# Kernel optimization log

Measured on AMD Instinct MI355X. Metric: run time of the kernel, lower is better.

## Reference

```python
import jax, jax.numpy as jnp
import numpy as np
from jax import lax

B, N_PROP, N_GT = 8, 8000, 256
NUM_CLASSES = 2
IMG_H = IMG_W = 800.0
FG_T = BG_T = 0.5            # Matcher thresholds
WX, WY, WW, WH = 10.0, 10.0, 5.0, 5.0  # BoxCoder weights
SCORE_T, NMS_T = 0.05, 0.5
PRE_NMS, DETS = 1000, 300     # boxes entering NMS, detections_per_img
DW_CLIP = float(np.log(1000.0 / 16.0))


def _rand_boxes(key, shape):
    k1, k2, k3, k4 = jax.random.split(key, 4)
    x1 = jax.random.uniform(k1, shape) * (IMG_W - 60.0)
    y1 = jax.random.uniform(k2, shape) * (IMG_H - 60.0)
    w = 10.0 + jax.random.uniform(k3, shape) * 250.0
    h = 10.0 + jax.random.uniform(k4, shape) * 250.0
    return jnp.stack([x1, y1, jnp.minimum(x1 + w, IMG_W), jnp.minimum(y1 + h, IMG_H)], -1)


def setup_inputs() -> dict:
    key = jax.random.key(0)
    kp, kg, kl, kb = jax.random.split(key, 4)
    n_all = N_PROP + N_GT
    return {
        "proposals": _rand_boxes(kp, (B, N_PROP)),
        "gt_boxes": _rand_boxes(kg, (B, N_GT)),
        "logits": jax.random.normal(kl, (B, n_all, NUM_CLASSES), jnp.float32),
        "box_regression": jax.random.normal(kb, (B, n_all, NUM_CLASSES * 4), jnp.float32) * 0.1,
    }


def box_iou(a, b):
    # a: [Na,4], b: [Nb,4] in xyxy -> [Na,Nb]
    area_a = (a[:, 2] - a[:, 0]) * (a[:, 3] - a[:, 1])
    area_b = (b[:, 2] - b[:, 0]) * (b[:, 3] - b[:, 1])
    lt = jnp.maximum(a[:, None, :2], b[None, :, :2])
    rb = jnp.minimum(a[:, None, 2:], b[None, :, 2:])
    wh = jnp.clip(rb - lt, 0.0)
    inter = wh[..., 0] * wh[..., 1]
    return inter / (area_a[:, None] + area_b[None, :] - inter)


def encode(ref_boxes, gt):
    # BoxCoder.encode, weights (10,10,5,5)
    pw = ref_boxes[:, 2] - ref_boxes[:, 0]
    ph = ref_boxes[:, 3] - ref_boxes[:, 1]
    pcx = ref_boxes[:, 0] + 0.5 * pw
    pcy = ref_boxes[:, 1] + 0.5 * ph
    gw = gt[:, 2] - gt[:, 0]
    gh = gt[:, 3] - gt[:, 1]
    gcx = gt[:, 0] + 0.5 * gw
    gcy = gt[:, 1] + 0.5 * gh
    return jnp.stack([
        WX * (gcx - pcx) / pw,
        WY * (gcy - pcy) / ph,
        WW * jnp.log(gw / pw),
        WH * jnp.log(gh / ph),
    ], -1)


def decode(rel, boxes):
    # rel: [N, C*4], boxes: [N,4] -> [N, C, 4]
    rel = rel.reshape(rel.shape[0], -1, 4)
    pw = boxes[:, 2] - boxes[:, 0]
    ph = boxes[:, 3] - boxes[:, 1]
    pcx = boxes[:, 0] + 0.5 * pw
    pcy = boxes[:, 1] + 0.5 * ph
    dx = rel[..., 0] / WX
    dy = rel[..., 1] / WY
    dw = jnp.minimum(rel[..., 2] / WW, DW_CLIP)
    dh = jnp.minimum(rel[..., 3] / WH, DW_CLIP)
    cx = dx * pw[:, None] + pcx[:, None]
    cy = dy * ph[:, None] + pcy[:, None]
    w = jnp.exp(dw) * pw[:, None]
    h = jnp.exp(dh) * ph[:, None]
    return jnp.stack([cx - 0.5 * w, cy - 0.5 * h, cx + 0.5 * w, cy + 0.5 * h], -1)


def _per_image(prop, gt, logit, breg):
    n_all = prop.shape[0] + gt.shape[0]
    prop_all = jnp.concatenate([prop, gt], 0)  # select_training_samples concat

    # --- assign_targets_to_proposals (Matcher) ---
    iou = box_iou(gt, prop_all)                 # [G, N_all]
    vals = iou.max(0)
    matches = iou.argmax(0)
    # gt_labels are all 1; bg -> 0, between thresholds -> -1 (empty when fg==bg)
    labels = jnp.where(vals < BG_T, 0, jnp.where(vals < FG_T, -1, 1))
    matched_gt = gt[matches]                    # [N_all, 4]
    reg_targets = encode(prop_all, matched_gt)  # [N_all, 4]

    # --- postprocess_detections ---
    pred = decode(breg, prop_all)               # [N_all, C, 4]
    boxes1 = pred[:, 1, :]                      # drop background class
    boxes1 = jnp.stack([
        jnp.clip(boxes1[:, 0], 0.0, IMG_W),
        jnp.clip(boxes1[:, 1], 0.0, IMG_H),
        jnp.clip(boxes1[:, 2], 0.0, IMG_W),
        jnp.clip(boxes1[:, 3], 0.0, IMG_H),
    ], -1)
    scores = jax.nn.softmax(logit, -1)[:, 1]
    sc = jnp.where(scores > SCORE_T, scores, -1.0)  # score_thresh filter

    top_s, top_i = lax.top_k(sc, PRE_NMS)
    top_b = boxes1[top_i]                       # [M, 4]
    ious = box_iou(top_b, top_b)                # [M, M]
    idx = jnp.arange(PRE_NMS)

    def body(keep, i):
        sup = (ious[i] > NMS_T) & keep[i] & (idx > i)
        return keep & ~sup, None

    keep, _ = lax.scan(body, jnp.ones(PRE_NMS, bool), idx)
    final = jnp.where(keep & (top_s > 0.0), top_s, -1.0)
    det_s, sel = lax.top_k(final, DETS)
    det_b = top_b[sel]
    return labels.astype(jnp.float32), reg_targets, det_b, det_s


def reference(proposals, gt_boxes, logits, box_regression):
    return jax.vmap(_per_image)(proposals, gt_boxes, logits, box_regression)
```

## Files before the change

kernel.cpp:

```cpp
#include <hip/hip_runtime.h>
#include <math.h>

#pragma clang fp contract(off)

#define BATCH 8
#define N_PROP 8000
#define N_GT 256
#define N_ALL 8256
#define PRE_NMS 1000
#define DETS 300
#define IMG 800.0f
#define DW_CLIP 4.135166556742356f
#define NWORDS 32
#define NBINS 8192
#define BIN_SCALE 8192.0f

__device__ __forceinline__ float exf(float x) { return (float)exp((double)x); }
__device__ __forceinline__ float lgf(float x) { return (float)log((double)x); }

__device__ __forceinline__ int score_bin(float s) {
  int b = (int)(s * BIN_SCALE);
  return (b < 0) ? 0 : (b > NBINS - 1 ? NBINS - 1 : b);
}

__device__ __forceinline__ int bxp(int j) { return j ^ ((j >> 5) & 7); }

#define REP32(F) F(0) F(1) F(2) F(3) F(4) F(5) F(6) F(7) F(8) F(9) F(10) \
  F(11) F(12) F(13) F(14) F(15) F(16) F(17) F(18) F(19) F(20) F(21) F(22) \
  F(23) F(24) F(25) F(26) F(27) F(28) F(29) F(30) F(31)


__global__ void __launch_bounds__(256)
prep_kernel(const float* __restrict__ prop,
            const float* __restrict__ gt,
            const float* __restrict__ logits,
            const float* __restrict__ breg,
            float* __restrict__ out_labels,
            float* __restrict__ out_regt,
            float* __restrict__ ws_boxes1,
            float* __restrict__ ws_sc) {
  const int b = blockIdx.y;
  const int tid = threadIdx.x;
  __shared__ __align__(16) float4 gsh4[N_GT];
  __shared__ float s_best[32];
  __shared__ int s_bi[32];
  {
    const float4* g4 = (const float4*)(gt + (size_t)b * N_GT * 4);
    gsh4[tid] = g4[tid];
  }
  __syncthreads();

  const int grp = tid >> 3;
  const int gl  = tid & 7;
  const int j = blockIdx.x * 32 + grp;

  float x1, y1, x2, y2;
  if (j < N_PROP) {
    const float4 p = ((const float4*)(prop + (size_t)b * N_PROP * 4))[j];
    x1 = p.x; y1 = p.y; x2 = p.z; y2 = p.w;
  } else {
    const float4 g = gsh4[j - N_PROP];
    x1 = g.x; y1 = g.y; x2 = g.z; y2 = g.w;
  }
  const float areaP = (x2 - x1) * (y2 - y1);

  float best = -1.0f; int bi = gl;
  #pragma unroll 4
  for (int t = 0; t < 32; ++t) {
    const int i = gl + (t << 3);
    const float4 g = gsh4[i];
    const float ga = (g.z - g.x) * (g.w - g.y);
    const float w = fmaxf(fminf(g.z, x2) - fmaxf(g.x, x1), 0.0f);
    const float h = fmaxf(fminf(g.w, y2) - fmaxf(g.y, y1), 0.0f);
    const float inter = w * h;
    const float iou = inter / (ga + areaP - inter);
    if (iou > best) { best = iou; bi = i; }
  }
  #pragma unroll
  for (int m = 1; m < 8; m <<= 1) {
    const float ov = __shfl_xor(best, m, 64);
    const int   oi = __shfl_xor(bi,  m, 64);
    if (ov > best || (ov == best && oi < bi)) { best = ov; bi = oi; }
  }
  if (gl == 0) { s_best[grp] = best; s_bi[grp] = bi; }
  __syncthreads();

  if (tid < 32) {
    const int j2 = blockIdx.x * 32 + tid;
    const float bst = s_best[tid];
    const int   gi  = s_bi[tid];

    float px1, py1, px2, py2;
    if (j2 < N_PROP) {
      const float4 p = ((const float4*)(prop + (size_t)b * N_PROP * 4))[j2];
      px1 = p.x; py1 = p.y; px2 = p.z; py2 = p.w;
    } else {
      const float4 g = gsh4[j2 - N_PROP];
      px1 = g.x; py1 = g.y; px2 = g.z; py2 = g.w;
    }

    out_labels[(size_t)b * N_ALL + j2] = (bst < 0.5f) ? 0.0f : 1.0f;

    const float pw = px2 - px1, ph = py2 - py1;
    const float pcx = px1 + 0.5f * pw, pcy = py1 + 0.5f * ph;
    const float4 gb = gsh4[gi];
    const float gw = gb.z - gb.x, gh = gb.w - gb.y;
    const float gcx = gb.x + 0.5f * gw, gcy = gb.y + 0.5f * gh;
    float4 rt;
    rt.x = 10.0f * (gcx - pcx) / pw;
    rt.y = 10.0f * (gcy - pcy) / ph;
    rt.z = 5.0f * lgf(gw / pw);
    rt.w = 5.0f * lgf(gh / ph);
    ((float4*)out_regt)[(size_t)b * N_ALL + j2] = rt;

    const float4 r = *(const float4*)(breg + (((size_t)b * N_ALL + j2) * 8 + 4));
    const float dx = r.x / 10.0f, dy = r.y / 10.0f;
    const float dw = fminf(r.z / 5.0f, DW_CLIP);
    const float dh = fminf(r.w / 5.0f, DW_CLIP);
    const float cx = dx * pw + pcx, cy = dy * ph + pcy;
    const float w2 = exf(dw) * pw, h2 = exf(dh) * ph;
    float4 bb;
    bb.x = fminf(fmaxf(cx - 0.5f * w2, 0.0f), IMG);
    bb.y = fminf(fmaxf(cy - 0.5f * h2, 0.0f), IMG);
    bb.z = fminf(fmaxf(cx + 0.5f * w2, 0.0f), IMG);
    bb.w = fminf(fmaxf(cy + 0.5f * h2, 0.0f), IMG);
    ((float4*)ws_boxes1)[(size_t)b * N_ALL + j2] = bb;

    const float2 lg = *(const float2*)(logits + ((size_t)b * N_ALL + j2) * 2);
    const float m = fmaxf(lg.x, lg.y);
    const float e0 = exf(lg.x - m), e1 = exf(lg.y - m);
    const float s = e1 / (e0 + e1);
    ws_sc[(size_t)b * N_ALL + j2] = (s > 0.05f) ? s : -1.0f;
  }
}

__global__ void __launch_bounds__(1024)
select_rank_kernel(const float* __restrict__ ws_sc,
                   const float* __restrict__ ws_boxes1,
                   float* __restrict__ top_s,
                   float* __restrict__ top_b) {
  const int b = blockIdx.x;
  const int tid = threadIdx.x;
  const int lane = tid & 63, wid = tid >> 6;
  __shared__ __align__(16) float ssc[N_ALL];
  __shared__ unsigned hist[NBINS];
  __shared__ __align__(16) float sc2[N_ALL];
  __shared__ unsigned short idx2[N_ALL];
  __shared__ int s_wt[16], s_wx[16];
  __shared__ int s_T, s_Nc;

  {
    const float4* g = (const float4*)(ws_sc + (size_t)b * N_ALL);
    float4* s4 = (float4*)ssc;
    float4 a0 = g[tid], a1 = g[tid + 1024];
    float4 a2 = make_float4(0.f, 0.f, 0.f, 0.f);
    const bool g2 = (tid + 2048) < (N_ALL / 4);
    if (g2) a2 = g[tid + 2048];
    s4[tid] = a0; s4[tid + 1024] = a1;
    if (g2) s4[tid + 2048] = a2;
  }
  #pragma unroll
  for (int i = 0; i < NBINS / 1024; ++i) hist[tid + i * 1024] = 0u;
  __syncthreads();
  for (int k = tid; k < N_ALL; k += 1024)
    atomicAdd(&hist[score_bin(ssc[k])], 1u);
  __syncthreads();

  int local = 0;
  #pragma unroll
  for (int i = 0; i < NBINS / 1024; ++i) local += (int)hist[tid * (NBINS / 1024) + i];

  int incl = local;
  #pragma unroll
  for (int off = 1; off < 64; off <<= 1) {
    const int u = __shfl_down(incl, off);
    incl += (lane + off < 64) ? u : 0;
  }
  if (lane == 0) s_wt[wid] = incl;
  __syncthreads();
  if (tid < 16) {
    const int v = s_wt[tid];
    int inc2 = v;
    #pragma unroll
    for (int off = 1; off < 16; off <<= 1) {
      const int u = __shfl_down(inc2, off);
      inc2 += (tid + off < 16) ? u : 0;
    }
    s_wx[tid] = inc2 - v;
  }
  __syncthreads();
  const int sa = (incl - local) + s_wx[wid];

  {
    int above = sa;
    const int hi = tid * (NBINS / 1024) + (NBINS / 1024) - 1;
    #pragma unroll
    for (int i = 0; i < NBINS / 1024; ++i) {
      const int bin = hi - i;
      const int c = (int)hist[bin];
      if (above < PRE_NMS && above + c >= PRE_NMS) { s_T = bin; s_Nc = above + c; }
      hist[bin] = (unsigned)above;
      above += c;
    }
  }
  __syncthreads();
  const int T = s_T;
  const int Nc = s_Nc;

  for (int k = tid; k < N_ALL; k += 1024) {
    const float v = ssc[k];
    const int bb = score_bin(v);
    if (bb >= T) {
      const int slot = (int)atomicAdd(&hist[bb], 1u);
      sc2[slot] = v;
      idx2[slot] = (unsigned short)k;
    }
  }
  __syncthreads();

  float* tsb = top_s + (size_t)b * PRE_NMS;
  float4* tbb = (float4*)top_b + (size_t)b * PRE_NMS;
  const float4* bx = (const float4*)ws_boxes1 + (size_t)b * N_ALL;
  for (int s = tid; s < Nc; s += 1024) {
    const float my = sc2[s];
    const int myb = score_bin(my);
    const int myi = (int)idx2[s];
    int gl = s;
    while (gl > 0 && score_bin(sc2[gl - 1]) == myb) --gl;
    int rank = gl;
    for (int k2 = gl; k2 < Nc; ++k2) {
      const float v = sc2[k2];
      if (score_bin(v) != myb) break;
      if (k2 == s) continue;
      rank += (int)((v > my) | ((v == my) & ((int)idx2[k2] < myi)));
    }
    if (rank < PRE_NMS) {
      tsb[rank] = my;
      tbb[rank] = bx[myi];
    }
  }
}

__global__ void mask_kernel(const float* __restrict__ top_b,
                            unsigned* __restrict__ ws_mask) {
  const int b = blockIdx.y;
  __shared__ __align__(16) float4 bx[PRE_NMS];
  const int tid = threadIdx.x;
  {
    const float4* gb = (const float4*)top_b + (size_t)b * PRE_NMS;
    float4 v0 = gb[tid], v1 = gb[tid + 256], v2 = gb[tid + 512];
    float4 v3 = make_float4(0.f, 0.f, 0.f, 0.f);
    const bool g3 = (tid + 768) < PRE_NMS;
    if (g3) v3 = gb[tid + 768];
    bx[bxp(tid)] = v0; bx[bxp(tid + 256)] = v1; bx[bxp(tid + 512)] = v2;
    if (g3) bx[bxp(tid + 768)] = v3;
  }
  __syncthreads();
  const int idx = blockIdx.x * blockDim.x + tid;
  if (idx >= PRE_NMS * NWORDS) return;
  const int i = idx >> 5;
  const int w = idx & 31;
  const float4 bi = bx[bxp(i)];
  const float ai = (bi.z - bi.x) * (bi.w - bi.y);
  unsigned bits = 0u;
  const int j0 = w * 32;
  #pragma unroll 8
  for (int jj = 0; jj < 32; ++jj) {
    const int j = j0 + jj;
    if (j > i && j < PRE_NMS) {
      const float4 bj = bx[bxp(j)];
      const float aj = (bj.z - bj.x) * (bj.w - bj.y);
      const float ww = fmaxf(fminf(bi.z, bj.z) - fmaxf(bi.x, bj.x), 0.0f);
      const float hh = fmaxf(fminf(bi.w, bj.w) - fmaxf(bi.y, bj.y), 0.0f);
      const float inter = ww * hh;
      const float iou = inter / (ai + aj - inter);
      if (iou > 0.5f) bits |= (1u << jj);
    }
  }
  ws_mask[((size_t)b * PRE_NMS + i) * NWORDS + w] = bits;
}

__global__ void __launch_bounds__(256)
scan_kernel(const unsigned* __restrict__ ws_mask,
            const float* __restrict__ top_s,
            const float* __restrict__ top_b,
            float* __restrict__ out_detb,
            float* __restrict__ out_dets) {
  const int b = blockIdx.x;
  const int tid = threadIdx.x;
  __shared__ __align__(16) unsigned smask[PRE_NMS * NWORDS];
  __shared__ int s_npos;
  __shared__ unsigned s_flw[NWORDS];
  __shared__ int s_pref[NWORDS + 1];
  const float* ts = top_s + (size_t)b * PRE_NMS;

  if (tid == 0) s_npos = 0;
  {
    const uint4* gm = (const uint4*)(ws_mask + (size_t)b * PRE_NMS * NWORDS);
    uint4* sm4 = (uint4*)smask;
    #pragma unroll
    for (int gs = 0; gs < 4; ++gs) {
      const int k0 = gs * 2048 + tid;
      uint4 t0 = gm[k0],        t1 = gm[k0 + 256],  t2 = gm[k0 + 512];
      uint4 t3 = gm[k0 + 768],  t4 = gm[k0 + 1024], t5 = gm[k0 + 1280];
      uint4 t6 = gm[k0 + 1536];
      uint4 t7 = make_uint4(0u, 0u, 0u, 0u);
      const bool g7 = (k0 + 1792) < (PRE_NMS * NWORDS / 4);
      if (g7) t7 = gm[k0 + 1792];
      sm4[k0] = t0;        sm4[k0 + 256] = t1;  sm4[k0 + 512] = t2;
      sm4[k0 + 768] = t3;  sm4[k0 + 1024] = t4; sm4[k0 + 1280] = t5;
      sm4[k0 + 1536] = t6;
      if (g7) sm4[k0 + 1792] = t7;
    }
  }
  int cnt = 0;
  for (int k = tid; k < PRE_NMS; k += 256) cnt += (ts[k] > 0.0f) ? 1 : 0;
  __syncthreads();
  if (cnt) atomicAdd(&s_npos, cnt);

  unsigned keep = 0u;
  if (tid < 64) {
    const int lane = tid;
    const int lw = lane & 31;
    keep = (lane < NWORDS) ? ((lane == 31) ? 0xFFu : 0xFFFFFFFFu) : 0u;
#define DECLA(J) unsigned rA##J;
    REP32(DECLA)
#undef DECLA
    for (int win = 0; win < 32; ++win) {
      const int base = win * 32;
#define LOADA(J) rA##J = smask[(base + J) * NWORDS + lw];
      REP32(LOADA)
#undef LOADA
      unsigned sw = (unsigned)__builtin_amdgcn_readlane((int)keep, win);
      unsigned sup = 0u;
#define STEPJ(J) { \
      const unsigned mJ = 0u - ((sw >> J) & 1u); \
      const unsigned rwJ = (unsigned)__builtin_amdgcn_readlane((int)rA##J, win); \
      sw &= ~(rwJ & mJ); \
      sup |= (rA##J & mJ); }
      REP32(STEPJ)
#undef STEPJ
      keep &= ~sup;
    }
  }
  __syncthreads();
  const int n_pos = s_npos;
  if (tid < NWORDS) {
    const int lo = tid * 32;
    int np = n_pos - lo;
    np = (np < 0) ? 0 : (np > 32 ? 32 : np);
    const unsigned npm = (np >= 32) ? 0xFFFFFFFFu : ((1u << np) - 1u);
    s_flw[tid] = keep & npm;
  }
  __syncthreads();
  if (tid == 0) {
    int s = 0;
    #pragma unroll
    for (int w = 0; w < NWORDS; ++w) { s_pref[w] = s; s += __popc(s_flw[w]); }
    s_pref[NWORDS] = s;
  }
  __syncthreads();
  const int tot = s_pref[NWORDS];

  for (int k = tid; k < PRE_NMS; k += 256) {
    const unsigned fw = s_flw[k >> 5];
    const int fbit = (int)((fw >> (k & 31)) & 1u);
    const int pos = s_pref[k >> 5] + __popc(fw & ((1u << (k & 31)) - 1u));
    int slot = -1; float sval = 0.0f;
    if (fbit) {
      if (pos < DETS) { slot = pos; sval = ts[k]; }
    } else {
      const int s2 = tot + (k - pos);
      if (s2 < DETS) { slot = s2; sval = -1.0f; }
    }
    if (slot >= 0) {
      out_dets[(size_t)b * DETS + slot] = sval;
      ((float4*)out_detb)[(size_t)b * DETS + slot] =
          ((const float4*)top_b)[(size_t)b * PRE_NMS + k];
    }
  }
}

extern "C" void kernel_launch(void* const* d_in, const int* in_sizes, int n_in,
                              void* d_out, int out_size, void* d_ws, size_t ws_size,
                              hipStream_t stream) {
  const float* prop   = (const float*)d_in[0];
  const float* gt     = (const float*)d_in[1];
  const float* logits = (const float*)d_in[2];
  const float* breg   = (const float*)d_in[3];

  float* out        = (float*)d_out;
  float* out_labels = out;
  float* out_regt   = out + (size_t)BATCH * N_ALL;
  float* out_detb   = out_regt + (size_t)BATCH * N_ALL * 4;
  float* out_dets   = out_detb + (size_t)BATCH * DETS * 4;

  float* ws_boxes1 = (float*)d_ws;
  float* ws_sc     = ws_boxes1 + (size_t)BATCH * N_ALL * 4;
  float* ws_tops   = ws_sc + (size_t)BATCH * N_ALL;
  float* ws_topb   = ws_tops + (size_t)BATCH * PRE_NMS;
  unsigned* ws_mask = (unsigned*)(ws_topb + (size_t)BATCH * PRE_NMS * 4);

  hipLaunchKernelGGL(prep_kernel, dim3(258, BATCH), dim3(256), 0, stream,
                     prop, gt, logits, breg, out_labels, out_regt, ws_boxes1, ws_sc);
  hipLaunchKernelGGL(select_rank_kernel, dim3(BATCH), dim3(1024), 0, stream,
                     ws_sc, ws_boxes1, ws_tops, ws_topb);
  dim3 gridm((PRE_NMS * NWORDS + 255) / 256, BATCH);
  hipLaunchKernelGGL(mask_kernel, gridm, dim3(256), 0, stream,
                     ws_topb, ws_mask);
  hipLaunchKernelGGL(scan_kernel, dim3(BATCH), dim3(256), 0, stream,
                     ws_mask, ws_tops, ws_topb, out_detb, out_dets);
}
```

Measured before the change: 65.09 us.

## Fuse score/decode into select kernel and co-schedule matcher with mask kernel

Softmax scoring moves into the select/rank kernel, and box decoding is done only for the top-ranked boxes there. This removes the prep kernel's full-size workspace writes and the separate launch. The matcher/encode work now runs as extra blocks inside the NMS mask kernel, so it overlaps with mask computation and drops another launch. The NMS scan also skips windows whose keep word is already zero. The cost is more serial work in the 8-block select kernel, which now reads the logits directly.

```diff
diff --git a/kernel.cpp b/kernel.cpp
--- a/kernel.cpp
+++ b/kernel.cpp
@@ -14,6 +14,8 @@
 #define NWORDS 32
 #define NBINS 8192
 #define BIN_SCALE 8192.0f
+#define MASK_BLOCKS 125
+#define PREP_BLOCKS 258
 
 __device__ __forceinline__ float exf(float x) { return (float)exp((double)x); }
 __device__ __forceinline__ float lgf(float x) { return (float)log((double)x); }
@@ -30,113 +32,11 @@
   F(23) F(24) F(25) F(26) F(27) F(28) F(29) F(30) F(31)
 
 
-__global__ void __launch_bounds__(256)
-prep_kernel(const float* __restrict__ prop,
-            const float* __restrict__ gt,
-            const float* __restrict__ logits,
-            const float* __restrict__ breg,
-            float* __restrict__ out_labels,
-            float* __restrict__ out_regt,
-            float* __restrict__ ws_boxes1,
-            float* __restrict__ ws_sc) {
-  const int b = blockIdx.y;
-  const int tid = threadIdx.x;
-  __shared__ __align__(16) float4 gsh4[N_GT];
-  __shared__ float s_best[32];
-  __shared__ int s_bi[32];
-  {
-    const float4* g4 = (const float4*)(gt + (size_t)b * N_GT * 4);
-    gsh4[tid] = g4[tid];
-  }
-  __syncthreads();
-
-  const int grp = tid >> 3;
-  const int gl  = tid & 7;
-  const int j = blockIdx.x * 32 + grp;
-
-  float x1, y1, x2, y2;
-  if (j < N_PROP) {
-    const float4 p = ((const float4*)(prop + (size_t)b * N_PROP * 4))[j];
-    x1 = p.x; y1 = p.y; x2 = p.z; y2 = p.w;
-  } else {
-    const float4 g = gsh4[j - N_PROP];
-    x1 = g.x; y1 = g.y; x2 = g.z; y2 = g.w;
-  }
-  const float areaP = (x2 - x1) * (y2 - y1);
-
-  float best = -1.0f; int bi = gl;
-  #pragma unroll 4
-  for (int t = 0; t < 32; ++t) {
-    const int i = gl + (t << 3);
-    const float4 g = gsh4[i];
-    const float ga = (g.z - g.x) * (g.w - g.y);
-    const float w = fmaxf(fminf(g.z, x2) - fmaxf(g.x, x1), 0.0f);
-    const float h = fmaxf(fminf(g.w, y2) - fmaxf(g.y, y1), 0.0f);
-    const float inter = w * h;
-    const float iou = inter / (ga + areaP - inter);
-    if (iou > best) { best = iou; bi = i; }
-  }
-  #pragma unroll
-  for (int m = 1; m < 8; m <<= 1) {
-    const float ov = __shfl_xor(best, m, 64);
-    const int   oi = __shfl_xor(bi,  m, 64);
-    if (ov > best || (ov == best && oi < bi)) { best = ov; bi = oi; }
-  }
-  if (gl == 0) { s_best[grp] = best; s_bi[grp] = bi; }
-  __syncthreads();
-
-  if (tid < 32) {
-    const int j2 = blockIdx.x * 32 + tid;
-    const float bst = s_best[tid];
-    const int   gi  = s_bi[tid];
-
-    float px1, py1, px2, py2;
-    if (j2 < N_PROP) {
-      const float4 p = ((const float4*)(prop + (size_t)b * N_PROP * 4))[j2];
-      px1 = p.x; py1 = p.y; px2 = p.z; py2 = p.w;
-    } else {
-      const float4 g = gsh4[j2 - N_PROP];
-      px1 = g.x; py1 = g.y; px2 = g.z; py2 = g.w;
-    }
-
-    out_labels[(size_t)b * N_ALL + j2] = (bst < 0.5f) ? 0.0f : 1.0f;
-
-    const float pw = px2 - px1, ph = py2 - py1;
-    const float pcx = px1 + 0.5f * pw, pcy = py1 + 0.5f * ph;
-    const float4 gb = gsh4[gi];
-    const float gw = gb.z - gb.x, gh = gb.w - gb.y;
-    const float gcx = gb.x + 0.5f * gw, gcy = gb.y + 0.5f * gh;
-    float4 rt;
-    rt.x = 10.0f * (gcx - pcx) / pw;
-    rt.y = 10.0f * (gcy - pcy) / ph;
-    rt.z = 5.0f * lgf(gw / pw);
-    rt.w = 5.0f * lgf(gh / ph);
-    ((float4*)out_regt)[(size_t)b * N_ALL + j2] = rt;
-
-    const float4 r = *(const float4*)(breg + (((size_t)b * N_ALL + j2) * 8 + 4));
-    const float dx = r.x / 10.0f, dy = r.y / 10.0f;
-    const float dw = fminf(r.z / 5.0f, DW_CLIP);
-    const float dh = fminf(r.w / 5.0f, DW_CLIP);
-    const float cx = dx * pw + pcx, cy = dy * ph + pcy;
-    const float w2 = exf(dw) * pw, h2 = exf(dh) * ph;
-    float4 bb;
-    bb.x = fminf(fmaxf(cx - 0.5f * w2, 0.0f), IMG);
-    bb.y = fminf(fmaxf(cy - 0.5f * h2, 0.0f), IMG);
-    bb.z = fminf(fmaxf(cx + 0.5f * w2, 0.0f), IMG);
-    bb.w = fminf(fmaxf(cy + 0.5f * h2, 0.0f), IMG);
-    ((float4*)ws_boxes1)[(size_t)b * N_ALL + j2] = bb;
-
-    const float2 lg = *(const float2*)(logits + ((size_t)b * N_ALL + j2) * 2);
-    const float m = fmaxf(lg.x, lg.y);
-    const float e0 = exf(lg.x - m), e1 = exf(lg.y - m);
-    const float s = e1 / (e0 + e1);
-    ws_sc[(size_t)b * N_ALL + j2] = (s > 0.05f) ? s : -1.0f;
-  }
-}
-
 __global__ void __launch_bounds__(1024)
-select_rank_kernel(const float* __restrict__ ws_sc,
-                   const float* __restrict__ ws_boxes1,
+select_rank_kernel(const float* __restrict__ prop,
+                   const float* __restrict__ gt,
+                   const float* __restrict__ logits,
+                   const float* __restrict__ breg,
                    float* __restrict__ top_s,
                    float* __restrict__ top_b) {
   const int b = blockIdx.x;
@@ -146,18 +46,18 @@
   __shared__ unsigned hist[NBINS];
   __shared__ __align__(16) float sc2[N_ALL];
   __shared__ unsigned short idx2[N_ALL];
+  __shared__ __align__(16) float4 gsh[N_GT];
   __shared__ int s_wt[16], s_wx[16];
   __shared__ int s_T, s_Nc;
 
-  {
-    const float4* g = (const float4*)(ws_sc + (size_t)b * N_ALL);
-    float4* s4 = (float4*)ssc;
-    float4 a0 = g[tid], a1 = g[tid + 1024];
-    float4 a2 = make_float4(0.f, 0.f, 0.f, 0.f);
-    const bool g2 = (tid + 2048) < (N_ALL / 4);
-    if (g2) a2 = g[tid + 2048];
-    s4[tid] = a0; s4[tid + 1024] = a1;
-    if (g2) s4[tid + 2048] = a2;
+  if (tid < N_GT) gsh[tid] = ((const float4*)(gt + (size_t)b * N_GT * 4))[tid];
+
+  for (int k = tid; k < N_ALL; k += 1024) {
+    const float2 lg = *(const float2*)(logits + ((size_t)b * N_ALL + k) * 2);
+    const float m = fmaxf(lg.x, lg.y);
+    const float e0 = exf(lg.x - m), e1 = exf(lg.y - m);
+    const float s = e1 / (e0 + e1);
+    ssc[k] = (s > 0.05f) ? s : -1.0f;
   }
   #pragma unroll
   for (int i = 0; i < NBINS / 1024; ++i) hist[tid + i * 1024] = 0u;
@@ -220,7 +120,6 @@
 
   float* tsb = top_s + (size_t)b * PRE_NMS;
   float4* tbb = (float4*)top_b + (size_t)b * PRE_NMS;
-  const float4* bx = (const float4*)ws_boxes1 + (size_t)b * N_ALL;
   for (int s = tid; s < Nc; s += 1024) {
     const float my = sc2[s];
     const int myb = score_bin(my);
@@ -236,48 +135,144 @@
     }
     if (rank < PRE_NMS) {
       tsb[rank] = my;
-      tbb[rank] = bx[myi];
+      float4 pb;
+      if (myi < N_PROP) pb = ((const float4*)(prop + (size_t)b * N_PROP * 4))[myi];
+      else              pb = gsh[myi - N_PROP];
+      const float pw = pb.z - pb.x, ph = pb.w - pb.y;
+      const float pcx = pb.x + 0.5f * pw, pcy = pb.y + 0.5f * ph;
+      const float4 r = *(const float4*)(breg + (((size_t)b * N_ALL + myi) * 8 + 4));
+      const float dx = r.x / 10.0f, dy = r.y / 10.0f;
+      const float dw = fminf(r.z / 5.0f, DW_CLIP);
+      const float dh = fminf(r.w / 5.0f, DW_CLIP);
+      const float cx = dx * pw + pcx, cy = dy * ph + pcy;
+      const float w2 = exf(dw) * pw, h2 = exf(dh) * ph;
+      float4 bb;
+      bb.x = fminf(fmaxf(cx - 0.5f * w2, 0.0f), IMG);
+      bb.y = fminf(fmaxf(cy - 0.5f * h2, 0.0f), IMG);
+      bb.z = fminf(fmaxf(cx + 0.5f * w2, 0.0f), IMG);
+      bb.w = fminf(fmaxf(cy + 0.5f * h2, 0.0f), IMG);
+      tbb[rank] = bb;
     }
   }
 }
 
-__global__ void mask_kernel(const float* __restrict__ top_b,
-                            unsigned* __restrict__ ws_mask) {
+__global__ void __launch_bounds__(256)
+mask_prep_kernel(const float* __restrict__ prop,
+                 const float* __restrict__ gt,
+                 const float* __restrict__ top_b,
+                 unsigned* __restrict__ ws_mask,
+                 float* __restrict__ out_labels,
+                 float* __restrict__ out_regt) {
   const int b = blockIdx.y;
+  const int tid = threadIdx.x;
   __shared__ __align__(16) float4 bx[PRE_NMS];
-  const int tid = threadIdx.x;
-  {
-    const float4* gb = (const float4*)top_b + (size_t)b * PRE_NMS;
-    float4 v0 = gb[tid], v1 = gb[tid + 256], v2 = gb[tid + 512];
-    float4 v3 = make_float4(0.f, 0.f, 0.f, 0.f);
-    const bool g3 = (tid + 768) < PRE_NMS;
-    if (g3) v3 = gb[tid + 768];
-    bx[bxp(tid)] = v0; bx[bxp(tid + 256)] = v1; bx[bxp(tid + 512)] = v2;
-    if (g3) bx[bxp(tid + 768)] = v3;
-  }
-  __syncthreads();
-  const int idx = blockIdx.x * blockDim.x + tid;
-  if (idx >= PRE_NMS * NWORDS) return;
-  const int i = idx >> 5;
-  const int w = idx & 31;
-  const float4 bi = bx[bxp(i)];
-  const float ai = (bi.z - bi.x) * (bi.w - bi.y);
-  unsigned bits = 0u;
-  const int j0 = w * 32;
-  #pragma unroll 8
-  for (int jj = 0; jj < 32; ++jj) {
-    const int j = j0 + jj;
-    if (j > i && j < PRE_NMS) {
-      const float4 bj = bx[bxp(j)];
-      const float aj = (bj.z - bj.x) * (bj.w - bj.y);
-      const float ww = fmaxf(fminf(bi.z, bj.z) - fmaxf(bi.x, bj.x), 0.0f);
-      const float hh = fmaxf(fminf(bi.w, bj.w) - fmaxf(bi.y, bj.y), 0.0f);
-      const float inter = ww * hh;
-      const float iou = inter / (ai + aj - inter);
-      if (iou > 0.5f) bits |= (1u << jj);
-    }
-  }
-  ws_mask[((size_t)b * PRE_NMS + i) * NWORDS + w] = bits;
+  __shared__ __align__(16) float4 gsh4[N_GT];
+  __shared__ float s_best[32];
+  __shared__ int s_bi[32];
+
+  if (blockIdx.x < MASK_BLOCKS) {
+    {
+      const float4* gb = (const float4*)top_b + (size_t)b * PRE_NMS;
+      float4 v0 = gb[tid], v1 = gb[tid + 256], v2 = gb[tid + 512];
+      float4 v3 = make_float4(0.f, 0.f, 0.f, 0.f);
+      const bool g3 = (tid + 768) < PRE_NMS;
+      if (g3) v3 = gb[tid + 768];
+      bx[bxp(tid)] = v0; bx[bxp(tid + 256)] = v1; bx[bxp(tid + 512)] = v2;
+      if (g3) bx[bxp(tid + 768)] = v3;
+    }
+    __syncthreads();
+    const int idx = blockIdx.x * 256 + tid;
+    const int i = idx >> 5;
+    const int w = idx & 31;
+    const float4 bi = bx[bxp(i)];
+    const float ai = (bi.z - bi.x) * (bi.w - bi.y);
+    unsigned bits = 0u;
+    const int j0 = w * 32;
+    #pragma unroll 8
+    for (int jj = 0; jj < 32; ++jj) {
+      const int j = j0 + jj;
+      if (j > i && j < PRE_NMS) {
+        const float4 bj = bx[bxp(j)];
+        const float aj = (bj.z - bj.x) * (bj.w - bj.y);
+        const float ww = fmaxf(fminf(bi.z, bj.z) - fmaxf(bi.x, bj.x), 0.0f);
+        const float hh = fmaxf(fminf(bi.w, bj.w) - fmaxf(bi.y, bj.y), 0.0f);
+        const float inter = ww * hh;
+        const float iou = inter / (ai + aj - inter);
+        if (iou > 0.5f) bits |= (1u << jj);
+      }
+    }
+    ws_mask[((size_t)b * PRE_NMS + i) * NWORDS + w] = bits;
+  } else {
+    {
+      const float4* g4 = (const float4*)(gt + (size_t)b * N_GT * 4);
+      gsh4[tid] = g4[tid];
+    }
+    __syncthreads();
+
+    const int grp = tid >> 3;
+    const int gl  = tid & 7;
+    const int j = (blockIdx.x - MASK_BLOCKS) * 32 + grp;
+
+    float x1, y1, x2, y2;
+    if (j < N_PROP) {
+      const float4 p = ((const float4*)(prop + (size_t)b * N_PROP * 4))[j];
+      x1 = p.x; y1 = p.y; x2 = p.z; y2 = p.w;
+    } else {
+      const float4 g = gsh4[j - N_PROP];
+      x1 = g.x; y1 = g.y; x2 = g.z; y2 = g.w;
+    }
+    const float areaP = (x2 - x1) * (y2 - y1);
+
+    float best = -1.0f; int bi = gl;
+    #pragma unroll 4
+    for (int t = 0; t < 32; ++t) {
+      const int i = gl + (t << 3);
+      const float4 g = gsh4[i];
+      const float ga = (g.z - g.x) * (g.w - g.y);
+      const float w = fmaxf(fminf(g.z, x2) - fmaxf(g.x, x1), 0.0f);
+      const float h = fmaxf(fminf(g.w, y2) - fmaxf(g.y, y1), 0.0f);
+      const float inter = w * h;
+      const float iou = inter / (ga + areaP - inter);
+      if (iou > best) { best = iou; bi = i; }
+    }
+    #pragma unroll
+    for (int m = 1; m < 8; m <<= 1) {
+      const float ov = __shfl_xor(best, m, 64);
+      const int   oi = __shfl_xor(bi,  m, 64);
+      if (ov > best || (ov == best && oi < bi)) { best = ov; bi = oi; }
+    }
+    if (gl == 0) { s_best[grp] = best; s_bi[grp] = bi; }
+    __syncthreads();
+
+    if (tid < 32) {
+      const int j2 = (blockIdx.x - MASK_BLOCKS) * 32 + tid;
+      const float bst = s_best[tid];
+      const int   gi  = s_bi[tid];
+
+      float px1, py1, px2, py2;
+      if (j2 < N_PROP) {
+        const float4 p = ((const float4*)(prop + (size_t)b * N_PROP * 4))[j2];
+        px1 = p.x; py1 = p.y; px2 = p.z; py2 = p.w;
+      } else {
+        const float4 g = gsh4[j2 - N_PROP];
+        px1 = g.x; py1 = g.y; px2 = g.z; py2 = g.w;
+      }
+
+      out_labels[(size_t)b * N_ALL + j2] = (bst < 0.5f) ? 0.0f : 1.0f;
+
+      const float pw = px2 - px1, ph = py2 - py1;
+      const float pcx = px1 + 0.5f * pw, pcy = py1 + 0.5f * ph;
+      const float4 gb = gsh4[gi];
+      const float gw = gb.z - gb.x, gh = gb.w - gb.y;
+      const float gcx = gb.x + 0.5f * gw, gcy = gb.y + 0.5f * gh;
+      float4 rt;
+      rt.x = 10.0f * (gcx - pcx) / pw;
+      rt.y = 10.0f * (gcy - pcy) / ph;
+      rt.z = 5.0f * lgf(gw / pw);
+      rt.w = 5.0f * lgf(gh / ph);
+      ((float4*)out_regt)[(size_t)b * N_ALL + j2] = rt;
+    }
+  }
 }
 
 __global__ void __launch_bounds__(256)
@@ -327,20 +322,22 @@
     REP32(DECLA)
 #undef DECLA
     for (int win = 0; win < 32; ++win) {
-      const int base = win * 32;
+      unsigned sw = (unsigned)__builtin_amdgcn_readlane((int)keep, win);
+      if (sw) {
+        const int base = win * 32;
 #define LOADA(J) rA##J = smask[(base + J) * NWORDS + lw];
-      REP32(LOADA)
+        REP32(LOADA)
 #undef LOADA
-      unsigned sw = (unsigned)__builtin_amdgcn_readlane((int)keep, win);
-      unsigned sup = 0u;
+        unsigned sup = 0u;
 #define STEPJ(J) { \
-      const unsigned mJ = 0u - ((sw >> J) & 1u); \
-      const unsigned rwJ = (unsigned)__builtin_amdgcn_readlane((int)rA##J, win); \
-      sw &= ~(rwJ & mJ); \
-      sup |= (rA##J & mJ); }
-      REP32(STEPJ)
+        const unsigned mJ = 0u - ((sw >> J) & 1u); \
+        const unsigned rwJ = (unsigned)__builtin_amdgcn_readlane((int)rA##J, win); \
+        sw &= ~(rwJ & mJ); \
+        sup |= (rA##J & mJ); }
+        REP32(STEPJ)
 #undef STEPJ
-      keep &= ~sup;
+        keep &= ~sup;
+      }
     }
   }
   __syncthreads();
@@ -395,19 +392,15 @@
   float* out_detb   = out_regt + (size_t)BATCH * N_ALL * 4;
   float* out_dets   = out_detb + (size_t)BATCH * DETS * 4;
 
-  float* ws_boxes1 = (float*)d_ws;
-  float* ws_sc     = ws_boxes1 + (size_t)BATCH * N_ALL * 4;
-  float* ws_tops   = ws_sc + (size_t)BATCH * N_ALL;
+  float* ws_tops   = (float*)d_ws;
   float* ws_topb   = ws_tops + (size_t)BATCH * PRE_NMS;
   unsigned* ws_mask = (unsigned*)(ws_topb + (size_t)BATCH * PRE_NMS * 4);
 
-  hipLaunchKernelGGL(prep_kernel, dim3(258, BATCH), dim3(256), 0, stream,
-                     prop, gt, logits, breg, out_labels, out_regt, ws_boxes1, ws_sc);
   hipLaunchKernelGGL(select_rank_kernel, dim3(BATCH), dim3(1024), 0, stream,
-                     ws_sc, ws_boxes1, ws_tops, ws_topb);
-  dim3 gridm((PRE_NMS * NWORDS + 255) / 256, BATCH);
-  hipLaunchKernelGGL(mask_kernel, gridm, dim3(256), 0, stream,
-                     ws_topb, ws_mask);
+                     prop, gt, logits, breg, ws_tops, ws_topb);
+  hipLaunchKernelGGL(mask_prep_kernel,
+                     dim3(MASK_BLOCKS + PREP_BLOCKS, BATCH), dim3(256), 0, stream,
+                     prop, gt, ws_topb, ws_mask, out_labels, out_regt);
   hipLaunchKernelGGL(scan_kernel, dim3(BATCH), dim3(256), 0, stream,
                      ws_mask, ws_tops, ws_topb, out_detb, out_dets);
 }
```

Result: slower. 66.63 us (+2.4%).
